# Kernel optimization log

Hardware: AMD Instinct MI355X
Metric: run time of the kernel (lower is better)

The kernel has to match this reference:

```python
import jax, jax.numpy as jnp
import numpy as np

NS, NT, D, H = 256, 16384, 3, 64
EPS = 1e-8  # smoothing_radius


def setup_inputs() -> dict:
    key = jax.random.key(0)
    ks = jax.random.split(key, 8)
    return {
        "reference_length": jnp.float32(1.0),
        "source_points": jax.random.normal(ks[0], (NS, D), jnp.float32),
        "target_points": jax.random.normal(ks[1], (NT, D), jnp.float32),
        "source_strengths": jax.random.normal(ks[2], (NS,), jnp.float32),
        "W1": jax.random.normal(ks[3], (1, H), jnp.float32),
        "b1": jnp.zeros((H,), jnp.float32),
        "pade_a": jax.random.normal(ks[4], (H, 3), jnp.float32) * 0.5,
        "pade_b": jax.random.normal(ks[5], (H, 2), jnp.float32) * 0.5,
        "W2": jax.random.normal(ks[6], (H, 2), jnp.float32) / jnp.sqrt(jnp.float32(H)),
        "b2": jnp.zeros((2,), jnp.float32),
    }


def reference(reference_length, source_points, target_points, source_strengths,
              W1, b1, pade_a, pade_b, W2, b2):
    # Pairwise relative positions: [T, S, D]
    r = target_points[:, None, :] - source_points[None, :, :]
    # Smoothed distance (smoothing_radius regularizes near r=0): [T, S]
    d = jnp.sqrt(jnp.sum(r * r, axis=-1) + EPS * EPS)
    # Dimensionless invariant feature: smoothed log-magnitude of r.
    # (With no source/global vectors, n_vectors_in=1 -> no SH pair features.)
    feat = jnp.log(d / reference_length)[..., None]            # [T, S, 1]
    # Pade rational network: linear -> per-channel rational activation -> linear
    x = feat @ W1 + b1                                          # [T, S, H]
    num = pade_a[:, 0] + pade_a[:, 1] * x + pade_a[:, 2] * x * x
    den = 1.0 + jnp.abs(pade_b[:, 0] * x + pade_b[:, 1] * x * x)
    h = num / den                                               # [T, S, H]
    out = h @ W2 + b2                                           # [T, S, 2]
    # Scatter (sum over sources) weighted by source strengths.
    scalar = jnp.einsum('ts,s->t', out[..., 0], source_strengths)      # [T]
    # Vector field: radial reprojection coefficient * unit r, summed over sources.
    r_hat = r / d[..., None]                                    # [T, S, D]
    vector = jnp.einsum('ts,tsd,s->td', out[..., 1], r_hat, source_strengths)
    # Pack scalar field 'phi' and vector field 'v' into one [T, 1+D] array.
    return jnp.concatenate([scalar[:, None], vector], axis=-1)
```

## Files before the change

### kernel.cpp

```cpp
#include <hip/hip_runtime.h>

#define NSRC 256
#define NTGT 16384
#define NH   64
#define TAB_N 3072
constexpr float TAB_LO = -10.0f;
constexpr float TAB_HI =  4.0f;
constexpr float TAB_STEP     = (TAB_HI - TAB_LO) / (float)TAB_N;
constexpr float TAB_INV_STEP = (float)TAB_N / (TAB_HI - TAB_LO);
constexpr float EPS2 = 1e-8f * 1e-8f;
constexpr float LN2  = 0.6931471805599453f;
constexpr int   TPB    = 256;
constexpr int   TGT_B  = 64;
constexpr int   NGRP   = 4;
constexpr int   SG     = NSRC / NGRP;

__global__ __launch_bounds__(256)
void build_table(const float* __restrict__ W1, const float* __restrict__ b1,
                 const float* __restrict__ pa, const float* __restrict__ pb,
                 const float* __restrict__ W2, float2* __restrict__ tab)
{
    const int i = blockIdx.x * 256 + threadIdx.x;
    if (i > TAB_N) return;
    const float feat = TAB_LO + (float)i * TAB_STEP;
    float g0 = 0.f, g1 = 0.f;
    for (int h = 0; h < NH; ++h) {
        const float x   = fmaf(feat, W1[h], b1[h]);
        const float x2  = x * x;
        const float num = fmaf(x2, pa[h * 3 + 2], fmaf(x, pa[h * 3 + 1], pa[h * 3 + 0]));
        const float den = 1.0f + fabsf(fmaf(x2, pb[h * 2 + 1], x * pb[h * 2 + 0]));
        const float g   = num * __builtin_amdgcn_rcpf(den);
        g0 = fmaf(g, W2[h * 2 + 0], g0);
        g1 = fmaf(g, W2[h * 2 + 1], g1);
    }
    tab[i] = make_float2(g0, g1);
}

__global__ __launch_bounds__(TPB)
void field_kernel(const float* __restrict__ refL,
                  const float* __restrict__ src,
                  const float* __restrict__ tgt,
                  const float* __restrict__ str,
                  const float* __restrict__ b2,
                  const float2* __restrict__ gtab,
                  float* __restrict__ out)
{
    __shared__ float4 tab[TAB_N];
    __shared__ float4 part[NGRP][TGT_B];

    for (int j = threadIdx.x; j < TAB_N; j += TPB) {
        const float2 a = gtab[j];
        const float2 b = gtab[j + 1];
        tab[j] = make_float4(a.x, a.y, b.x, b.y);
    }
    __syncthreads();

    const int jt = threadIdx.x & (TGT_B - 1);
    const int g  = __builtin_amdgcn_readfirstlane(threadIdx.x >> 6);
    const int t  = blockIdx.x * TGT_B + jt;
    const int sb = g * SG;

    const float tx = tgt[t * 3 + 0];
    const float ty = tgt[t * 3 + 1];
    const float tz = tgt[t * 3 + 2];
    const float logL = __builtin_amdgcn_logf(refL[0]) * LN2;
    const float K1 = 0.5f * LN2 * TAB_INV_STEP;
    const float K2 = (-logL - TAB_LO) * TAB_INV_STEP;
    const float b20 = b2[0], b21 = b2[1];

    float acc0 = 0.f, ax = 0.f, ay = 0.f, az = 0.f;
    #pragma unroll 16
    for (int i = 0; i < SG; ++i) {
        const int s = sb + i;
        const float rx = tx - src[s * 3 + 0];
        const float ry = ty - src[s * 3 + 1];
        const float rz = tz - src[s * 3 + 2];
        const float d2 = fmaf(rx, rx, fmaf(ry, ry, fmaf(rz, rz, EPS2)));
        const float idxf = fmaf(__builtin_amdgcn_logf(d2), K1, K2);
        int ii = (int)floorf(idxf);
        ii = min(max(ii, 0), TAB_N - 1);
        const float frac = idxf - (float)ii;
        const float4 e = tab[ii];
        const float g0 = fmaf(frac, e.z - e.x, e.x);
        const float g1 = fmaf(frac, e.w - e.y, e.y);
        const float invd = __builtin_amdgcn_rsqf(d2);
        const float w = str[s];
        acc0 = fmaf(g0 + b20, w, acc0);
        const float c = (g1 + b21) * w * invd;
        ax = fmaf(c, rx, ax);
        ay = fmaf(c, ry, ay);
        az = fmaf(c, rz, az);
    }

    part[g][jt] = make_float4(acc0, ax, ay, az);
    __syncthreads();

    if (threadIdx.x < TGT_B) {
        const float4 p0 = part[0][jt];
        const float4 p1 = part[1][jt];
        const float4 p2 = part[2][jt];
        const float4 p3 = part[3][jt];
        float4 r;
        r.x = (p0.x + p1.x) + (p2.x + p3.x);
        r.y = (p0.y + p1.y) + (p2.y + p3.y);
        r.z = (p0.z + p1.z) + (p2.z + p3.z);
        r.w = (p0.w + p1.w) + (p2.w + p3.w);
        ((float4*)out)[t] = r;
    }
}

extern "C" void kernel_launch(void* const* d_in, const int* in_sizes, int n_in,
                              void* d_out, int out_size, void* d_ws, size_t ws_size,
                              hipStream_t stream) {
    const float* refL = (const float*)d_in[0];
    const float* src  = (const float*)d_in[1];
    const float* tgt  = (const float*)d_in[2];
    const float* str  = (const float*)d_in[3];
    const float* W1   = (const float*)d_in[4];
    const float* b1   = (const float*)d_in[5];
    const float* pa   = (const float*)d_in[6];
    const float* pb   = (const float*)d_in[7];
    const float* W2   = (const float*)d_in[8];
    const float* b2   = (const float*)d_in[9];
    float*  out  = (float*)d_out;
    float2* gtab = (float2*)d_ws;

    build_table<<<dim3((TAB_N + 256) / 256), dim3(256), 0, stream>>>(
        W1, b1, pa, pb, W2, gtab);

    field_kernel<<<dim3(NTGT / TGT_B), dim3(TPB), 0, stream>>>(
        refL, src, tgt, str, b2, gtab, out);
}
```

Baseline: 89.53 us.

## Prebuild interleaved float4 table with folded bias and double source-split groups

After: 84.94 us. 1.05x faster.

```diff
diff --git a/kernel.cpp b/kernel.cpp
--- a/kernel.cpp
+++ b/kernel.cpp
@@ -4,26 +4,27 @@
 #define NTGT 16384
 #define NH   64
 #define TAB_N 3072
-constexpr float TAB_LO = -10.0f;
-constexpr float TAB_HI =  4.0f;
+constexpr float TAB_LO = -7.0f;
+constexpr float TAB_HI =  3.0f;
 constexpr float TAB_STEP     = (TAB_HI - TAB_LO) / (float)TAB_N;
 constexpr float TAB_INV_STEP = (float)TAB_N / (TAB_HI - TAB_LO);
 constexpr float EPS2 = 1e-8f * 1e-8f;
 constexpr float LN2  = 0.6931471805599453f;
-constexpr int   TPB    = 256;
+constexpr int   TPB    = 512;
 constexpr int   TGT_B  = 64;
-constexpr int   NGRP   = 4;
+constexpr int   NGRP   = 8;
 constexpr int   SG     = NSRC / NGRP;
 
 __global__ __launch_bounds__(256)
 void build_table(const float* __restrict__ W1, const float* __restrict__ b1,
                  const float* __restrict__ pa, const float* __restrict__ pb,
-                 const float* __restrict__ W2, float2* __restrict__ tab)
+                 const float* __restrict__ W2, const float* __restrict__ b2,
+                 float4* __restrict__ tab4)
 {
     const int i = blockIdx.x * 256 + threadIdx.x;
     if (i > TAB_N) return;
     const float feat = TAB_LO + (float)i * TAB_STEP;
-    float g0 = 0.f, g1 = 0.f;
+    float g0 = b2[0], g1 = b2[1];
     for (int h = 0; h < NH; ++h) {
         const float x   = fmaf(feat, W1[h], b1[h]);
         const float x2  = x * x;
@@ -33,7 +34,9 @@
         g0 = fmaf(g, W2[h * 2 + 0], g0);
         g1 = fmaf(g, W2[h * 2 + 1], g1);
     }
-    tab[i] = make_float2(g0, g1);
+    float2* t2 = (float2*)tab4;
+    if (i < TAB_N) t2[2 * i + 0] = make_float2(g0, g1);
+    if (i > 0)     t2[2 * i - 1] = make_float2(g0, g1);
 }
 
 __global__ __launch_bounds__(TPB)
@@ -41,18 +44,13 @@
                   const float* __restrict__ src,
                   const float* __restrict__ tgt,
                   const float* __restrict__ str,
-                  const float* __restrict__ b2,
-                  const float2* __restrict__ gtab,
+                  const float4* __restrict__ gtab,
                   float* __restrict__ out)
 {
     __shared__ float4 tab[TAB_N];
     __shared__ float4 part[NGRP][TGT_B];
 
-    for (int j = threadIdx.x; j < TAB_N; j += TPB) {
-        const float2 a = gtab[j];
-        const float2 b = gtab[j + 1];
-        tab[j] = make_float4(a.x, a.y, b.x, b.y);
-    }
+    for (int j = threadIdx.x; j < TAB_N; j += TPB) tab[j] = gtab[j];
     __syncthreads();
 
     const int jt = threadIdx.x & (TGT_B - 1);
@@ -66,7 +64,6 @@
     const float logL = __builtin_amdgcn_logf(refL[0]) * LN2;
     const float K1 = 0.5f * LN2 * TAB_INV_STEP;
     const float K2 = (-logL - TAB_LO) * TAB_INV_STEP;
-    const float b20 = b2[0], b21 = b2[1];
 
     float acc0 = 0.f, ax = 0.f, ay = 0.f, az = 0.f;
     #pragma unroll 16
@@ -85,8 +82,8 @@
         const float g1 = fmaf(frac, e.w - e.y, e.y);
         const float invd = __builtin_amdgcn_rsqf(d2);
         const float w = str[s];
-        acc0 = fmaf(g0 + b20, w, acc0);
-        const float c = (g1 + b21) * w * invd;
+        acc0 = fmaf(g0, w, acc0);
+        const float c = g1 * w * invd;
         ax = fmaf(c, rx, ax);
         ay = fmaf(c, ry, ay);
         az = fmaf(c, rz, az);
@@ -96,15 +93,12 @@
     __syncthreads();
 
     if (threadIdx.x < TGT_B) {
-        const float4 p0 = part[0][jt];
-        const float4 p1 = part[1][jt];
-        const float4 p2 = part[2][jt];
-        const float4 p3 = part[3][jt];
-        float4 r;
-        r.x = (p0.x + p1.x) + (p2.x + p3.x);
-        r.y = (p0.y + p1.y) + (p2.y + p3.y);
-        r.z = (p0.z + p1.z) + (p2.z + p3.z);
-        r.w = (p0.w + p1.w) + (p2.w + p3.w);
+        float4 r = part[0][jt];
+        #pragma unroll
+        for (int k = 1; k < NGRP; ++k) {
+            const float4 p = part[k][jt];
+            r.x += p.x; r.y += p.y; r.z += p.z; r.w += p.w;
+        }
         ((float4*)out)[t] = r;
     }
 }
@@ -123,11 +117,11 @@
     const float* W2   = (const float*)d_in[8];
     const float* b2   = (const float*)d_in[9];
     float*  out  = (float*)d_out;
-    float2* gtab = (float2*)d_ws;
+    float4* tab4 = (float4*)d_ws;
 
     build_table<<<dim3((TAB_N + 256) / 256), dim3(256), 0, stream>>>(
-        W1, b1, pa, pb, W2, gtab);
+        W1, b1, pa, pb, W2, b2, tab4);
 
     field_kernel<<<dim3(NTGT / TGT_B), dim3(TPB), 0, stream>>>(
-        refL, src, tgt, str, b2, gtab, out);
+        refL, src, tgt, str, tab4, out);
 }
```
